# Performance work log

Hardware: AMD Instinct MI355X
Metric: run time of the kernel (lower is better)

The kernel has to match this reference:

```python
import jax, jax.numpy as jnp
import numpy as np

B, T, C = 4, 2048, 1024
H = 16
HD = C // H


def setup_inputs() -> dict:
    key = jax.random.key(0)
    k1, k2, k3 = jax.random.split(key, 3)
    x = jax.random.normal(k1, (B, T, C), dtype=jnp.float32)
    w_qkv = jax.random.normal(k2, (C, 3 * C), dtype=jnp.float32) * (C ** -0.5)
    w_proj = jax.random.normal(k3, (C, C), dtype=jnp.float32) * (C ** -0.5)
    b_proj = jnp.zeros((C,), dtype=jnp.float32)
    return {"x": x, "w_qkv": w_qkv, "w_proj": w_proj, "b_proj": b_proj}


def reference(x, w_qkv, w_proj, b_proj):
    Bd, Td, Cd = x.shape
    scale = HD ** -0.5
    qkv = x @ w_qkv  # [B,T,3C]
    q, k, v = jnp.split(qkv, 3, axis=-1)
    # [B,H,T,HD]
    q = q.reshape(Bd, Td, H, HD).transpose(0, 2, 1, 3)
    k = k.reshape(Bd, Td, H, HD).transpose(0, 2, 1, 3)
    v = v.reshape(Bd, Td, H, HD).transpose(0, 2, 1, 3)
    att = jnp.einsum('bhqd,bhkd->bhqk', q, k) * scale
    causal = jnp.triu(jnp.ones((Td, Td), dtype=bool), k=1)
    att = jnp.where(causal, -jnp.inf, att)
    att = jax.nn.softmax(att, axis=-1)
    y = jnp.einsum('bhqk,bhkd->bhqd', att, v)
    y = y.transpose(0, 2, 1, 3).reshape(Bd, Td, Cd)
    return y @ w_proj + b_proj
```

## Files before the change

### kernel.cpp

```cpp
#include <hip/hip_runtime.h>

typedef unsigned short u16;
typedef __attribute__((ext_vector_type(8))) short short8;
typedef __attribute__((ext_vector_type(4))) short short4v;
typedef __attribute__((ext_vector_type(4))) float floatx4;
typedef __attribute__((ext_vector_type(4))) unsigned short ushort4v;

#define B_ 4
#define T_ 2048
#define C_ 1024
#define H_ 16
#define HD_ 64

template <bool V> struct BC { static constexpr bool value = V; };
template <int N> struct ICN { static constexpr int v = N; };

static __device__ __forceinline__ u16 f2bf(float f) {
  union { float f; unsigned int i; } c; c.f = f;
  unsigned int u = c.i;
  return (u16)((u + 0x7FFFu + ((u >> 16) & 1u)) >> 16);
}
static __device__ __forceinline__ unsigned pk2(float lo, float hi) {
  union { float f; unsigned u; } a, b; a.f = hi; b.f = lo;
  return __builtin_amdgcn_perm(a.u, b.u, 0x07060302u);
}
static __device__ __forceinline__ unsigned pk2r(float lo, float hi) {
  return (unsigned)f2bf(lo) | ((unsigned)f2bf(hi) << 16);
}

static __device__ __forceinline__ void gload16(const u16* g, u16* l) {
  __builtin_amdgcn_global_load_lds(
      (const __attribute__((address_space(1))) unsigned int*)(g),
      (__attribute__((address_space(3))) unsigned int*)(l), 16, 0, 0);
}

__global__ __launch_bounds__(256) void prep_k(const float* __restrict__ x,
                                              const float* __restrict__ w_qkv,
                                              const float* __restrict__ w_proj,
                                              u16* __restrict__ xbf,
                                              u16* __restrict__ wqkvT,
                                              u16* __restrict__ wprojT) {
  const int bid = blockIdx.x;
  if (bid < 8192) {
    const int i = bid * 256 + threadIdx.x;
    const float4 f = ((const float4*)x)[i];
    ushort4v o;
    o.x = f2bf(f.x); o.y = f2bf(f.y); o.z = f2bf(f.z); o.w = f2bf(f.w);
    *(ushort4v*)(xbf + (size_t)i * 4) = o;
    return;
  }
  __shared__ u16 tile[32][33];
  const float* in;
  u16* out;
  int R, Cc, tb;
  if (bid < 11264) {
    in = w_qkv; out = wqkvT; R = C_; Cc = 3 * C_; tb = bid - 8192;
  } else {
    in = w_proj; out = wprojT; R = C_; Cc = C_; tb = bid - 11264;
  }
  const int tpr = Cc / 32;
  const int bx = (tb % tpr) * 32;
  const int by = (tb / tpr) * 32;
  const int tx = threadIdx.x & 31;
  const int ty = threadIdx.x >> 5;
  #pragma unroll
  for (int i = ty; i < 32; i += 8)
    tile[i][tx] = f2bf(in[(size_t)(by + i) * Cc + bx + tx]);
  __syncthreads();
  #pragma unroll
  for (int i = ty; i < 32; i += 8)
    out[(size_t)(bx + i) * R + by + tx] = tile[tx][i];
}

template <int MODE>
__global__ __launch_bounds__(512, 1)
void gemm8x(const u16* __restrict__ A, const u16* __restrict__ Bt,
            u16* __restrict__ outb, u16* __restrict__ outv,
            float* __restrict__ outf, const float* __restrict__ bias,
            int N) {
  constexpr int ABUF = 8192;
  constexpr int BBUF = 16384;
  constexpr int BUF = ABUF + BBUF;
  __shared__ __align__(16) u16 lds[2 * BUF];

  const int bid = blockIdx.x;
  const int xcd = bid & 7;
  const int loc = bid >> 3;
  const int tM = (xcd * 8 + (loc & 7)) * 128;
  const int tN = (loc >> 3) * 256;
  const int tid = threadIdx.x;
  const int wave = tid >> 6;
  const int lane = tid & 63;
  const int lr = lane & 15;
  const int quad = lane >> 4;
  const int wm = wave >> 2;
  const int wn = wave & 3;
  const int csw = (lr >> 1) & 3;
  const int srow = lane >> 2;
  const int skofs = ((lane & 3) ^ ((lane >> 3) & 3)) * 8;

  const u16* gA  = A  + (size_t)(tM + wave * 16 + srow) * 1024 + skofs;
  const u16* gB0 = Bt + (size_t)(tN + (wave * 2) * 16 + srow) * 1024 + skofs;
  const u16* gB1 = Bt + (size_t)(tN + (wave * 2 + 1) * 16 + srow) * 1024 + skofs;
  u16* lA  = &lds[wave * 512];
  u16* lB0 = &lds[ABUF + (wave * 2) * 512];
  u16* lB1 = &lds[ABUF + (wave * 2 + 1) * 512];

  const floatx4 zf = {0.f, 0.f, 0.f, 0.f};
  floatx4 acc[4][4];
  #pragma unroll
  for (int i = 0; i < 4; i++)
    #pragma unroll
    for (int j = 0; j < 4; j++) acc[i][j] = zf;

  auto stage = [&](int t, int kh) {
    const int buf = t & 1;
    const int go = t * 64 + kh * 32;
    gload16(gA + go,  lA  + buf * BUF + kh * 4096);
    gload16(gB0 + go, lB0 + buf * BUF + kh * 8192);
    gload16(gB1 + go, lB1 + buf * BUF + kh * 8192);
  };

  auto phase = [&](int t, int kh, auto STG, auto VM) {
    const int buf = t & 1;
    const u16* pA = &lds[buf * BUF + kh * 4096];
    const u16* pB = &lds[buf * BUF + ABUF + kh * 8192];
    short8 af[4], bf[4];
    #pragma unroll
    for (int mt = 0; mt < 4; mt++)
      af[mt] = *(const short8*)(&pA[(wm * 64 + mt * 16 + lr) * 32 + ((quad ^ csw) * 8)]);
    #pragma unroll
    for (int nt = 0; nt < 4; nt++)
      bf[nt] = *(const short8*)(&pB[(wn * 64 + nt * 16 + lr) * 32 + ((quad ^ csw) * 8)]);
    if constexpr (decltype(STG)::value) stage(t + 1, kh);
    asm volatile("s_barrier" ::: "memory");
    asm volatile("s_waitcnt lgkmcnt(0)" ::: "memory");
    __builtin_amdgcn_sched_barrier(0);
    __builtin_amdgcn_s_setprio(1);
    #pragma unroll
    for (int mt = 0; mt < 4; mt++)
      #pragma unroll
      for (int nt = 0; nt < 4; nt++)
        acc[mt][nt] = __builtin_amdgcn_mfma_f32_16x16x32_bf16(af[mt], bf[nt],
                                                              acc[mt][nt], 0, 0, 0);
    __builtin_amdgcn_s_setprio(0);
    constexpr int vm = decltype(VM)::v;
    if constexpr (vm == 3)
      asm volatile("s_waitcnt vmcnt(3)\n\ts_barrier" ::: "memory");
    else if constexpr (vm == 0)
      asm volatile("s_waitcnt vmcnt(0)\n\ts_barrier" ::: "memory");
    else
      asm volatile("s_barrier" ::: "memory");
  };

  stage(0, 0);
  stage(0, 1);
  asm volatile("s_waitcnt vmcnt(3)\n\ts_barrier" ::: "memory");

  #pragma unroll 1
  for (int t = 0; t < 15; t++) {
    phase(t, 0, BC<true>{}, ICN<3>{});
    phase(t, 1, BC<true>{}, ICN<3>{});
  }
  phase(15, 0, BC<false>{}, ICN<0>{});
  phase(15, 1, BC<false>{}, ICN<-1>{});

  if constexpr (MODE == 1) {
    if (tN >= 2 * C_) {
      #pragma unroll
      for (int mt = 0; mt < 4; mt++) {
        const int t0 = wm * 64 + mt * 16 + quad * 4;
        #pragma unroll
        for (int nt = 0; nt < 4; nt++) {
          const int vrow = wn * 64 + nt * 16 + lr;
          u16* p = &lds[vrow * 128 + (((t0 >> 3) ^ (vrow & 7)) * 8) + (t0 & 7)];
          *(unsigned*)(p)     = pk2r(acc[mt][nt][0], acc[mt][nt][1]);
          *(unsigned*)(p + 2) = pk2r(acc[mt][nt][2], acc[mt][nt][3]);
        }
      }
      asm volatile("s_waitcnt lgkmcnt(0)\n\ts_barrier" ::: "memory");
      const int b = tM >> 11;
      const int t0b = tM & (T_ - 1);
      const int h0 = (tN - 2 * C_) >> 6;
      u16* vb = outv + (size_t)(b * H_ + h0) * HD_ * T_;
      #pragma unroll
      for (int i = 0; i < 8; i++) {
        const int lin = tid + i * 512;
        const int row = lin >> 4;
        const int chv = lin & 15;
        const short8 v = *(const short8*)(&lds[row * 128 + ((chv ^ (row & 7)) * 8)]);
        *(short8*)(vb + (size_t)row * T_ + t0b + chv * 8) = v;
      }
      return;
    }
    #pragma unroll
    for (int mt = 0; mt < 4; mt++) {
      const int m0 = tM + wm * 64 + mt * 16 + quad * 4;
      #pragma unroll
      for (int nt = 0; nt < 4; nt++) {
        const int n = tN + wn * 64 + nt * 16 + lr;
        #pragma unroll
        for (int r = 0; r < 4; r++)
          outb[(size_t)(m0 + r) * N + n] = f2bf(acc[mt][nt][r]);
      }
    }
  } else {
    #pragma unroll
    for (int mt = 0; mt < 4; mt++) {
      const int m0 = tM + wm * 64 + mt * 16 + quad * 4;
      #pragma unroll
      for (int nt = 0; nt < 4; nt++) {
        const int n = tN + wn * 64 + nt * 16 + lr;
        const float bv = bias[n];
        #pragma unroll
        for (int r = 0; r < 4; r++)
          __builtin_nontemporal_store(acc[mt][nt][r] + bv,
                                      &outf[(size_t)(m0 + r) * N + n]);
      }
    }
  }
}

__global__ __launch_bounds__(256, 4) void attn_k(const u16* __restrict__ qkv,
                                                 const u16* __restrict__ vt,
                                                 u16* __restrict__ y) {
  __shared__ __align__(16) u16 Ks[64 * 64];
  __shared__ __align__(16) u16 Vs[64 * 64];
  const int bid = blockIdx.x;
  const int s = bid >> 3;
  const int qp = s >> 3;
  const int bh = ((s & 7) << 3) | (bid & 7);
  const int b = bh >> 4, h = bh & 15;
  const int tid = threadIdx.x;
  const int wave = tid >> 6;
  const int lane = tid & 63;
  const int lr = lane & 15;
  const int quad = lane >> 4;
  const int qtA = qp, qtB = 31 - qp;

  const int srow = lane >> 3;
  const int skofs = ((lane & 7) ^ ((lane >> 3) & 7)) * 8;
  const int gsw = lr & 7;

  const size_t RS = 3 * C_;
  const u16* qcol = qkv + (size_t)b * T_ * RS + h * HD_;
  const u16* kcol = qcol + C_;

  const size_t qrA = (size_t)(qtA * 64 + wave * 16 + lr) * RS;
  const size_t qrB = (size_t)(qtB * 64 + wave * 16 + lr) * RS;
  const short8 aq0A = *(const short8*)(qcol + qrA + quad * 8);
  const short8 aq1A = *(const short8*)(qcol + qrA + 32 + quad * 8);
  const short8 aq0B = *(const short8*)(qcol + qrB + quad * 8);
  const short8 aq1B = *(const short8*)(qcol + qrB + 32 + quad * 8);

  const floatx4 zf = {0.f, 0.f, 0.f, 0.f};
  const float C1 = 0.125f * 1.44269504f;
  const float C2 = -16.0f * 1.44269504f;
  const short8 vones = {16256, 16256, 16256, 16256, 16256, 16256, 16256, 16256};

  floatx4 accA[4], accB[4];
  floatx4 accSA = zf, accSB = zf;
  #pragma unroll
  for (int i = 0; i < 4; i++) { accA[i] = zf; accB[i] = zf; }

  auto stage = [&](int kt) {
    __syncthreads();
    #pragma unroll
    for (int j = 0; j < 2; j++) {
      const int seg = wave * 2 + j;
      const int row = seg * 8 + srow;
      gload16(kcol + (size_t)(kt * 64 + row) * RS + skofs, &Ks[seg * 512]);
      gload16(vt + ((size_t)bh * HD_ + row) * T_ + kt * 64 + skofs, &Vs[seg * 512]);
    }
    __syncthreads();
  };

  auto core = [&](auto WA, auto DA, auto DB) {
    constexpr bool wA = decltype(WA)::value;
    constexpr bool dA = decltype(DA)::value;
    constexpr bool dB = decltype(DB)::value;
    float peA[4][4], peB[4][4];
    #pragma unroll
    for (int nt = 0; nt < 4; nt++) {
      const short8 bk0 =
          *(const short8*)(&Ks[(nt * 16 + lr) * 64 + ((quad ^ gsw) * 8)]);
      const short8 bk1 =
          *(const short8*)(&Ks[(nt * 16 + lr) * 64 + (((quad + 4) ^ gsw) * 8)]);
      {
        floatx4 st = __builtin_amdgcn_mfma_f32_16x16x32_bf16(
            bk1, aq1B,
            __builtin_amdgcn_mfma_f32_16x16x32_bf16(bk0, aq0B, zf, 0, 0, 0),
            0, 0, 0);
        #pragma unroll
        for (int r = 0; r < 4; r++) {
          float pe = __builtin_amdgcn_exp2f(fmaf(st[r], C1, C2));
          if constexpr (dB)
            if (nt * 16 + quad * 4 + r > wave * 16 + lr) pe = 0.f;
          peB[nt][r] = pe;
        }
      }
      if constexpr (wA) {
        floatx4 st = __builtin_amdgcn_mfma_f32_16x16x32_bf16(
            bk1, aq1A,
            __builtin_amdgcn_mfma_f32_16x16x32_bf16(bk0, aq0A, zf, 0, 0, 0),
            0, 0, 0);
        #pragma unroll
        for (int r = 0; r < 4; r++) {
          float pe = __builtin_amdgcn_exp2f(fmaf(st[r], C1, C2));
          if constexpr (dA)
            if (nt * 16 + quad * 4 + r > wave * 16 + lr) pe = 0.f;
          peA[nt][r] = pe;
        }
      }
    }

    short8 pB[2], pA[2];
    #pragma unroll
    for (int h2 = 0; h2 < 2; h2++) {
      union { unsigned u[4]; short8 s8; } w;
      w.u[0] = pk2(peB[2 * h2][0], peB[2 * h2][1]);
      w.u[1] = pk2(peB[2 * h2][2], peB[2 * h2][3]);
      w.u[2] = pk2(peB[2 * h2 + 1][0], peB[2 * h2 + 1][1]);
      w.u[3] = pk2(peB[2 * h2 + 1][2], peB[2 * h2 + 1][3]);
      pB[h2] = w.s8;
    }
    if constexpr (wA) {
      #pragma unroll
      for (int h2 = 0; h2 < 2; h2++) {
        union { unsigned u[4]; short8 s8; } w;
        w.u[0] = pk2(peA[2 * h2][0], peA[2 * h2][1]);
        w.u[1] = pk2(peA[2 * h2][2], peA[2 * h2][3]);
        w.u[2] = pk2(peA[2 * h2 + 1][0], peA[2 * h2 + 1][1]);
        w.u[3] = pk2(peA[2 * h2 + 1][2], peA[2 * h2 + 1][3]);
        pA[h2] = w.s8;
      }
    }

    #pragma unroll
    for (int h2 = 0; h2 < 2; h2++) {
      accSB = __builtin_amdgcn_mfma_f32_16x16x32_bf16(vones, pB[h2], accSB, 0, 0, 0);
      if constexpr (wA)
        accSA = __builtin_amdgcn_mfma_f32_16x16x32_bf16(vones, pA[h2], accSA, 0, 0, 0);
      #pragma unroll
      for (int dt = 0; dt < 4; dt++) {
        const int base = (dt * 16 + lr) * 64;
        const int cl = h2 * 4 + (quad >> 1);
        const int off_lo = ((cl ^ gsw) * 8) + (quad & 1) * 4;
        const int off_hi = (((cl + 2) ^ gsw) * 8) + (quad & 1) * 4;
        const short4v vlo = *(const short4v*)(&Vs[base + off_lo]);
        const short4v vhi = *(const short4v*)(&Vs[base + off_hi]);
        const short8 av = __builtin_shufflevector(vlo, vhi, 0, 1, 2, 3, 4, 5, 6, 7);
        accB[dt] = __builtin_amdgcn_mfma_f32_16x16x32_bf16(av, pB[h2], accB[dt], 0, 0, 0);
        if constexpr (wA)
          accA[dt] = __builtin_amdgcn_mfma_f32_16x16x32_bf16(av, pA[h2], accA[dt], 0, 0, 0);
      }
    }
  };

  for (int kt = 0; kt < qtA; kt++) { stage(kt); core(BC<true>{}, BC<false>{}, BC<false>{}); }
  stage(qtA); core(BC<true>{}, BC<true>{}, BC<false>{});
  for (int kt = qtA + 1; kt < qtB; kt++) { stage(kt); core(BC<false>{}, BC<false>{}, BC<false>{}); }
  stage(qtB); core(BC<false>{}, BC<false>{}, BC<true>{});

  #pragma unroll
  for (int ph = 0; ph < 2; ph++) {
    const int qt = ph ? qtB : qtA;
    const floatx4* acc = ph ? accB : accA;
    const float inv = 1.f / (ph ? accSB[0] : accSA[0]);
    const int qg = qt * 64 + wave * 16 + lr;
    u16* yrow = y + ((size_t)(b * T_ + qg)) * C_ + h * HD_;
    #pragma unroll
    for (int dt = 0; dt < 4; dt++) {
      ushort4v o;
      #pragma unroll
      for (int r = 0; r < 4; r++) o[r] = f2bf(acc[dt][r] * inv);
      *(ushort4v*)(yrow + dt * 16 + quad * 4) = o;
    }
  }
}

extern "C" void kernel_launch(void* const* d_in, const int* in_sizes, int n_in,
                              void* d_out, int out_size, void* d_ws, size_t ws_size,
                              hipStream_t stream) {
  const float* x      = (const float*)d_in[0];
  const float* w_qkv  = (const float*)d_in[1];
  const float* w_proj = (const float*)d_in[2];
  const float* b_proj = (const float*)d_in[3];
  float* out = (float*)d_out;

  u16* ws = (u16*)d_ws;
  const size_t SZ = (size_t)B_ * T_ * C_;
  u16* xbf    = ws;
  u16* wqkvT  = xbf + SZ;
  u16* wprojT = wqkvT + (size_t)3 * C_ * C_;
  u16* qkvw   = wprojT + (size_t)C_ * C_;
  u16* vtw    = qkvw + 3 * SZ;
  u16* yw     = xbf;

  prep_k<<<12288, 256, 0, stream>>>(x, w_qkv, w_proj, xbf, wqkvT, wprojT);
  gemm8x<1><<<768, 512, 0, stream>>>(
      xbf, wqkvT, qkvw, vtw, nullptr, nullptr, 3 * C_);
  attn_k<<<1024, 256, 0, stream>>>(qkvw, vtw, yw);
  gemm8x<2><<<256, 512, 0, stream>>>(
      yw, wprojT, nullptr, nullptr, out, b_proj, C_);
}
```

Before: 231.1 us.

## Deepen GEMM LDS pipeline to four stages and double-buffer attention K/V tiles

The GEMM now stages 32-wide K slices into a 4-deep LDS ring, prefetching three slices ahead. It also reads register fragments for the next slice while the MFMAs for the current slice run, with one barrier per slice instead of two per phase. The attention kernel double-buffers its K and V tiles so the next tile's global-to-LDS loads overlap the current tile's compute, replacing two __syncthreads per tile with one waitcnt plus barrier. This doubles attention LDS use, which may reduce occupancy, and holds more fragment registers in the GEMM.

New measurement: 231.6 us. About the same (+0.2%).

```diff
diff --git a/kernel.cpp b/kernel.cpp
--- a/kernel.cpp
+++ b/kernel.cpp
@@ -13,7 +13,6 @@
 #define HD_ 64
 
 template <bool V> struct BC { static constexpr bool value = V; };
-template <int N> struct ICN { static constexpr int v = N; };
 
 static __device__ __forceinline__ u16 f2bf(float f) {
   union { float f; unsigned int i; } c; c.f = f;
@@ -74,14 +73,14 @@
 
 template <int MODE>
 __global__ __launch_bounds__(512, 1)
-void gemm8x(const u16* __restrict__ A, const u16* __restrict__ Bt,
+void gemmrp(const u16* __restrict__ A, const u16* __restrict__ Bt,
             u16* __restrict__ outb, u16* __restrict__ outv,
             float* __restrict__ outf, const float* __restrict__ bias,
             int N) {
-  constexpr int ABUF = 8192;
-  constexpr int BBUF = 16384;
+  constexpr int ABUF = 4096;
+  constexpr int BBUF = 8192;
   constexpr int BUF = ABUF + BBUF;
-  __shared__ __align__(16) u16 lds[2 * BUF];
+  __shared__ __align__(16) u16 lds[4 * BUF];
 
   const int bid = blockIdx.x;
   const int xcd = bid & 7;
@@ -100,11 +99,8 @@
   const int skofs = ((lane & 3) ^ ((lane >> 3) & 3)) * 8;
 
   const u16* gA  = A  + (size_t)(tM + wave * 16 + srow) * 1024 + skofs;
-  const u16* gB0 = Bt + (size_t)(tN + (wave * 2) * 16 + srow) * 1024 + skofs;
-  const u16* gB1 = Bt + (size_t)(tN + (wave * 2 + 1) * 16 + srow) * 1024 + skofs;
-  u16* lA  = &lds[wave * 512];
-  u16* lB0 = &lds[ABUF + (wave * 2) * 512];
-  u16* lB1 = &lds[ABUF + (wave * 2 + 1) * 512];
+  const u16* gB0 = Bt + (size_t)(tN + wave * 32 + srow) * 1024 + skofs;
+  const u16* gB1 = Bt + (size_t)(tN + wave * 32 + 16 + srow) * 1024 + skofs;
 
   const floatx4 zf = {0.f, 0.f, 0.f, 0.f};
   floatx4 acc[4][4];
@@ -113,29 +109,26 @@
     #pragma unroll
     for (int j = 0; j < 4; j++) acc[i][j] = zf;
 
-  auto stage = [&](int t, int kh) {
-    const int buf = t & 1;
-    const int go = t * 64 + kh * 32;
-    gload16(gA + go,  lA  + buf * BUF + kh * 4096);
-    gload16(gB0 + go, lB0 + buf * BUF + kh * 8192);
-    gload16(gB1 + go, lB1 + buf * BUF + kh * 8192);
+  auto stage = [&](int t) {
+    const int buf = t & 3;
+    const int go = t * 32;
+    gload16(gA + go,  &lds[buf * BUF + wave * 512]);
+    gload16(gB0 + go, &lds[buf * BUF + ABUF + wave * 1024]);
+    gload16(gB1 + go, &lds[buf * BUF + ABUF + wave * 1024 + 512]);
   };
 
-  auto phase = [&](int t, int kh, auto STG, auto VM) {
-    const int buf = t & 1;
-    const u16* pA = &lds[buf * BUF + kh * 4096];
-    const u16* pB = &lds[buf * BUF + ABUF + kh * 8192];
-    short8 af[4], bf[4];
+  auto readf = [&](int t, short8 (&af)[4], short8 (&bf)[4]) {
+    const u16* pA = &lds[(t & 3) * BUF];
+    const u16* pB = pA + ABUF;
     #pragma unroll
     for (int mt = 0; mt < 4; mt++)
       af[mt] = *(const short8*)(&pA[(wm * 64 + mt * 16 + lr) * 32 + ((quad ^ csw) * 8)]);
     #pragma unroll
     for (int nt = 0; nt < 4; nt++)
       bf[nt] = *(const short8*)(&pB[(wn * 64 + nt * 16 + lr) * 32 + ((quad ^ csw) * 8)]);
-    if constexpr (decltype(STG)::value) stage(t + 1, kh);
-    asm volatile("s_barrier" ::: "memory");
-    asm volatile("s_waitcnt lgkmcnt(0)" ::: "memory");
-    __builtin_amdgcn_sched_barrier(0);
+  };
+
+  auto mfma16 = [&](short8 (&af)[4], short8 (&bf)[4]) {
     __builtin_amdgcn_s_setprio(1);
     #pragma unroll
     for (int mt = 0; mt < 4; mt++)
@@ -144,26 +137,44 @@
         acc[mt][nt] = __builtin_amdgcn_mfma_f32_16x16x32_bf16(af[mt], bf[nt],
                                                               acc[mt][nt], 0, 0, 0);
     __builtin_amdgcn_s_setprio(0);
-    constexpr int vm = decltype(VM)::v;
-    if constexpr (vm == 3)
-      asm volatile("s_waitcnt vmcnt(3)\n\ts_barrier" ::: "memory");
-    else if constexpr (vm == 0)
-      asm volatile("s_waitcnt vmcnt(0)\n\ts_barrier" ::: "memory");
-    else
-      asm volatile("s_barrier" ::: "memory");
   };
 
-  stage(0, 0);
-  stage(0, 1);
+  short8 afc[4], bfc[4], afn[4], bfn[4];
+
+  stage(0); stage(1); stage(2);
   asm volatile("s_waitcnt vmcnt(3)\n\ts_barrier" ::: "memory");
+  readf(0, afc, bfc);
 
   #pragma unroll 1
-  for (int t = 0; t < 15; t++) {
-    phase(t, 0, BC<true>{}, ICN<3>{});
-    phase(t, 1, BC<true>{}, ICN<3>{});
-  }
-  phase(15, 0, BC<false>{}, ICN<0>{});
-  phase(15, 1, BC<false>{}, ICN<-1>{});
+  for (int t = 0; t < 28; t += 2) {
+    readf(t + 1, afn, bfn);
+    stage(t + 3);
+    __builtin_amdgcn_sched_barrier(0);
+    mfma16(afc, bfc);
+    __builtin_amdgcn_sched_barrier(0);
+    asm volatile("s_waitcnt vmcnt(3)\n\ts_barrier" ::: "memory");
+    readf(t + 2, afc, bfc);
+    stage(t + 4);
+    __builtin_amdgcn_sched_barrier(0);
+    mfma16(afn, bfn);
+    __builtin_amdgcn_sched_barrier(0);
+    asm volatile("s_waitcnt vmcnt(3)\n\ts_barrier" ::: "memory");
+  }
+  readf(29, afn, bfn);
+  stage(31);
+  __builtin_amdgcn_sched_barrier(0);
+  mfma16(afc, bfc);
+  __builtin_amdgcn_sched_barrier(0);
+  asm volatile("s_waitcnt vmcnt(3)\n\ts_barrier" ::: "memory");
+  readf(30, afc, bfc);
+  __builtin_amdgcn_sched_barrier(0);
+  mfma16(afn, bfn);
+  __builtin_amdgcn_sched_barrier(0);
+  asm volatile("s_waitcnt vmcnt(0)\n\ts_barrier" ::: "memory");
+  readf(31, afn, bfn);
+  __builtin_amdgcn_sched_barrier(0);
+  mfma16(afc, bfc);
+  mfma16(afn, bfn);
 
   if constexpr (MODE == 1) {
     if (tN >= 2 * C_) {
@@ -224,8 +235,8 @@
 __global__ __launch_bounds__(256, 4) void attn_k(const u16* __restrict__ qkv,
                                                  const u16* __restrict__ vt,
                                                  u16* __restrict__ y) {
-  __shared__ __align__(16) u16 Ks[64 * 64];
-  __shared__ __align__(16) u16 Vs[64 * 64];
+  __shared__ __align__(16) u16 Ks[2 * 4096];
+  __shared__ __align__(16) u16 Vs[2 * 4096];
   const int bid = blockIdx.x;
   const int s = bid >> 3;
   const int qp = s >> 3;
@@ -263,29 +274,30 @@
   #pragma unroll
   for (int i = 0; i < 4; i++) { accA[i] = zf; accB[i] = zf; }
 
-  auto stage = [&](int kt) {
-    __syncthreads();
+  auto stage = [&](int kt, int buf) {
     #pragma unroll
     for (int j = 0; j < 2; j++) {
       const int seg = wave * 2 + j;
       const int row = seg * 8 + srow;
-      gload16(kcol + (size_t)(kt * 64 + row) * RS + skofs, &Ks[seg * 512]);
-      gload16(vt + ((size_t)bh * HD_ + row) * T_ + kt * 64 + skofs, &Vs[seg * 512]);
-    }
-    __syncthreads();
+      gload16(kcol + (size_t)(kt * 64 + row) * RS + skofs, &Ks[buf * 4096 + seg * 512]);
+      gload16(vt + ((size_t)bh * HD_ + row) * T_ + kt * 64 + skofs, &Vs[buf * 4096 + seg * 512]);
+    }
+    __builtin_amdgcn_sched_barrier(0);
   };
 
-  auto core = [&](auto WA, auto DA, auto DB) {
+  auto core = [&](int cur, auto WA, auto DA, auto DB) {
     constexpr bool wA = decltype(WA)::value;
     constexpr bool dA = decltype(DA)::value;
     constexpr bool dB = decltype(DB)::value;
+    const u16* Kb = &Ks[cur * 4096];
+    const u16* Vb = &Vs[cur * 4096];
     float peA[4][4], peB[4][4];
     #pragma unroll
     for (int nt = 0; nt < 4; nt++) {
       const short8 bk0 =
-          *(const short8*)(&Ks[(nt * 16 + lr) * 64 + ((quad ^ gsw) * 8)]);
+          *(const short8*)(&Kb[(nt * 16 + lr) * 64 + ((quad ^ gsw) * 8)]);
       const short8 bk1 =
-          *(const short8*)(&Ks[(nt * 16 + lr) * 64 + (((quad + 4) ^ gsw) * 8)]);
+          *(const short8*)(&Kb[(nt * 16 + lr) * 64 + (((quad + 4) ^ gsw) * 8)]);
       {
         floatx4 st = __builtin_amdgcn_mfma_f32_16x16x32_bf16(
             bk1, aq1B,
@@ -347,8 +359,8 @@
         const int cl = h2 * 4 + (quad >> 1);
         const int off_lo = ((cl ^ gsw) * 8) + (quad & 1) * 4;
         const int off_hi = (((cl + 2) ^ gsw) * 8) + (quad & 1) * 4;
-        const short4v vlo = *(const short4v*)(&Vs[base + off_lo]);
-        const short4v vhi = *(const short4v*)(&Vs[base + off_hi]);
+        const short4v vlo = *(const short4v*)(&Vb[base + off_lo]);
+        const short4v vhi = *(const short4v*)(&Vb[base + off_hi]);
         const short8 av = __builtin_shufflevector(vlo, vhi, 0, 1, 2, 3, 4, 5, 6, 7);
         accB[dt] = __builtin_amdgcn_mfma_f32_16x16x32_bf16(av, pB[h2], accB[dt], 0, 0, 0);
         if constexpr (wA)
@@ -357,10 +369,26 @@
     }
   };
 
-  for (int kt = 0; kt < qtA; kt++) { stage(kt); core(BC<true>{}, BC<false>{}, BC<false>{}); }
-  stage(qtA); core(BC<true>{}, BC<true>{}, BC<false>{});
-  for (int kt = qtA + 1; kt < qtB; kt++) { stage(kt); core(BC<false>{}, BC<false>{}, BC<false>{}); }
-  stage(qtB); core(BC<false>{}, BC<false>{}, BC<true>{});
+  stage(0, 0);
+  asm volatile("s_waitcnt vmcnt(0)\n\ts_barrier" ::: "memory");
+  int cur = 0;
+  for (int kt = 0; kt < qtA; kt++) {
+    stage(kt + 1, cur ^ 1);
+    core(cur, BC<true>{}, BC<false>{}, BC<false>{});
+    asm volatile("s_waitcnt vmcnt(0)\n\ts_barrier" ::: "memory");
+    cur ^= 1;
+  }
+  stage(qtA + 1, cur ^ 1);
+  core(cur, BC<true>{}, BC<true>{}, BC<false>{});
+  asm volatile("s_waitcnt vmcnt(0)\n\ts_barrier" ::: "memory");
+  cur ^= 1;
+  for (int kt = qtA + 1; kt < qtB; kt++) {
+    stage(kt + 1, cur ^ 1);
+    core(cur, BC<false>{}, BC<false>{}, BC<false>{});
+    asm volatile("s_waitcnt vmcnt(0)\n\ts_barrier" ::: "memory");
+    cur ^= 1;
+  }
+  core(cur, BC<false>{}, BC<false>{}, BC<true>{});
 
   #pragma unroll
   for (int ph = 0; ph < 2; ph++) {
@@ -398,9 +426,9 @@
   u16* yw     = xbf;
 
   prep_k<<<12288, 256, 0, stream>>>(x, w_qkv, w_proj, xbf, wqkvT, wprojT);
-  gemm8x<1><<<768, 512, 0, stream>>>(
+  gemmrp<1><<<768, 512, 0, stream>>>(
       xbf, wqkvT, qkvw, vtw, nullptr, nullptr, 3 * C_);
   attn_k<<<1024, 256, 0, stream>>>(qkvw, vtw, yw);
-  gemm8x<2><<<256, 512, 0, stream>>>(
+  gemmrp<2><<<256, 512, 0, stream>>>(
       yw, wprojT, nullptr, nullptr, out, b_proj, C_);
 }
```
